# Optimization experiments

Measured on AMD Instinct MI355X. Metric: run time of the kernel, lower is better.

The kernel has to match this reference:

```python
import jax, jax.numpy as jnp
import numpy as np

D_MODEL = 1024
NUM_HEADS = 16
D_K = D_MODEL // NUM_HEADS


def setup_inputs() -> dict:
    key = jax.random.key(0)
    ks = jax.random.split(key, 7)
    B, S = 2, 2048
    scale = 1.0 / np.sqrt(D_MODEL)
    return {
        "Q": jax.random.normal(ks[0], (B, S, D_MODEL), dtype=jnp.float32),
        "K": jax.random.normal(ks[1], (B, S, D_MODEL), dtype=jnp.float32),
        "V": jax.random.normal(ks[2], (B, S, D_MODEL), dtype=jnp.float32),
        "W_q": jax.random.normal(ks[3], (D_MODEL, D_MODEL), dtype=jnp.float32) * scale,
        "W_k": jax.random.normal(ks[4], (D_MODEL, D_MODEL), dtype=jnp.float32) * scale,
        "W_v": jax.random.normal(ks[5], (D_MODEL, D_MODEL), dtype=jnp.float32) * scale,
        "W_o": jax.random.normal(ks[6], (D_MODEL, D_MODEL), dtype=jnp.float32) * scale,
    }


def _split_heads(x):
    B, S, _ = x.shape
    return x.reshape(B, S, NUM_HEADS, D_K).transpose(0, 2, 1, 3)  # [B,H,S,Dk]


def reference(Q, K, V, W_q, W_k, W_v, W_o):
    # nn.Linear(bias=False): x @ W.T
    q = _split_heads(Q @ W_q.T)
    k = _split_heads(K @ W_k.T)
    v = _split_heads(V @ W_v.T)
    scores = jnp.einsum("bhqd,bhkd->bhqk", q, k) / jnp.sqrt(jnp.float32(D_K))
    probs = jax.nn.softmax(scores, axis=-1)
    out = jnp.einsum("bhqk,bhkd->bhqd", probs, v)  # [B,H,S,Dk]
    B, H, S, Dk = out.shape
    out = out.transpose(0, 2, 1, 3).reshape(B, S, H * Dk)
    return out @ W_o.T
```

## Files before the change

### kernel.cpp

```cpp
#include <hip/hip_runtime.h>
#include <cstdint>

#define D_MODEL 1024
#define NH 16
#define DK 64
#define SEQ 2048
#define BATCH 2
#define M_TOT (BATCH * SEQ)

typedef __bf16 bf16x8          __attribute__((ext_vector_type(8)));
typedef unsigned short u16x8   __attribute__((ext_vector_type(8)));
typedef float  f32x4           __attribute__((ext_vector_type(4)));

union pun8 { u16x8 u; bf16x8 b; };

__device__ __forceinline__ f32x4 mfma16(bf16x8 a, bf16x8 b, f32x4 c) {
    return __builtin_amdgcn_mfma_f32_16x16x32_bf16(a, b, c, 0, 0, 0);
}

__device__ __forceinline__ unsigned short f2bf(float f) {
    union { float f; uint32_t u; } v; v.f = f;
    uint32_t u = v.u;
    return (unsigned short)((u + 0x7FFFu + ((u >> 16) & 1u)) >> 16);
}

__device__ __forceinline__ unsigned short f2bf_trunc(float f) {
    union { float f; uint32_t u; } v; v.f = f;
    return (unsigned short)(v.u >> 16);
}

__device__ __forceinline__ void gl_lds16(const unsigned short* g, unsigned short* l) {
    __builtin_amdgcn_global_load_lds(
        (const __attribute__((address_space(1))) void*)g,
        (__attribute__((address_space(3))) void*)l, 16, 0, 0);
}

#define C_EXP2 0.1803368801111204f

__global__ __launch_bounds__(256) void convert_all_kernel(
    const float* __restrict__ Q,  const float* __restrict__ K,
    const float* __restrict__ V,  const float* __restrict__ Wq,
    const float* __restrict__ Wk, const float* __restrict__ Wv,
    const float* __restrict__ Wo,
    unsigned short* __restrict__ Qb,  unsigned short* __restrict__ Kb,
    unsigned short* __restrict__ Vb,  unsigned short* __restrict__ Wqb,
    unsigned short* __restrict__ Wkb, unsigned short* __restrict__ Wvb,
    unsigned short* __restrict__ Wob)
{
    int bid = blockIdx.x;
    const float* src; unsigned short* dst; int base;
    if (bid < 3 * 2048) {
        int r = bid >> 11;
        src  = (r == 0) ? Q  : (r == 1) ? K  : V;
        dst  = (r == 0) ? Qb : (r == 1) ? Kb : Vb;
        base = (bid & 2047) * 2048;
    } else {
        int u = bid - 3 * 2048;
        int r = u >> 9;
        src  = (r == 0) ? Wq  : (r == 1) ? Wk  : (r == 2) ? Wv  : Wo;
        dst  = (r == 0) ? Wqb : (r == 1) ? Wkb : (r == 2) ? Wvb : Wob;
        base = (u & 511) * 2048;
    }
    int i = base + threadIdx.x * 8;
    float4 a = *(const float4*)(src + i);
    float4 b = *(const float4*)(src + i + 4);
    u16x8 o;
    o[0] = f2bf(a.x); o[1] = f2bf(a.y); o[2] = f2bf(a.z); o[3] = f2bf(a.w);
    o[4] = f2bf(b.x); o[5] = f2bf(b.y); o[6] = f2bf(b.z); o[7] = f2bf(b.w);
    *(u16x8*)(dst + i) = o;
}

__global__ __launch_bounds__(256) void qkv_proj_kernel(
    const unsigned short* __restrict__ Q,
    const unsigned short* __restrict__ K,
    const unsigned short* __restrict__ V,
    const unsigned short* __restrict__ Wq,
    const unsigned short* __restrict__ Wk,
    const unsigned short* __restrict__ Wv,
    unsigned short* __restrict__ qb,
    unsigned short* __restrict__ kb,
    unsigned short* __restrict__ vtb)
{
    const int z = blockIdx.z;
    const unsigned short* A  = (z == 0) ? Q  : (z == 1) ? K  : V;
    const unsigned short* Bt = (z == 0) ? Wq : (z == 1) ? Wk : Wv;

    const int m0 = blockIdx.y * 128;
    const int n0 = blockIdx.x * 128;

    __shared__ __align__(16) unsigned short smem[128 * 136];
    unsigned short* As = smem;
    unsigned short* Bs = smem + 128 * 64;
    unsigned short* Cs = smem;

    const int t    = threadIdx.x;
    const int lane = t & 63;
    const int w    = t >> 6;
    const int l15  = lane & 15;
    const int quad = lane >> 4;
    const int wm   = (w >> 1) * 64;
    const int wn   = (w & 1) * 64;

    f32x4 acc[4][4] = {};

    for (int k0 = 0; k0 < D_MODEL; k0 += 64) {
        __syncthreads();
        #pragma unroll
        for (int i = 0; i < 4; i++) {
            int u   = t + i * 256;
            int row = u >> 3;
            int kc  = (u & 7) * 8;
            gl_lds16(&A [(m0 + row) * D_MODEL + k0 + kc], &As[(i * 256 + w * 64) * 8]);
            gl_lds16(&Bt[(n0 + row) * D_MODEL + k0 + kc], &Bs[(i * 256 + w * 64) * 8]);
        }
        __syncthreads();

        #pragma unroll
        for (int kk = 0; kk < 2; kk++) {
            bf16x8 a[4], b[4];
            #pragma unroll
            for (int mi = 0; mi < 4; mi++)
                a[mi] = *(const bf16x8*)(&As[(wm + mi * 16 + l15) * 64 + kk * 32 + quad * 8]);
            #pragma unroll
            for (int ni = 0; ni < 4; ni++)
                b[ni] = *(const bf16x8*)(&Bs[(wn + ni * 16 + l15) * 64 + kk * 32 + quad * 8]);

            #pragma unroll
            for (int mi = 0; mi < 4; mi++)
                #pragma unroll
                for (int ni = 0; ni < 4; ni++)
                    acc[mi][ni] = mfma16(a[mi], b[ni], acc[mi][ni]);
        }
    }

    const float oscale = (z == 0) ? C_EXP2 : 1.0f;
    __syncthreads();
    #pragma unroll
    for (int mi = 0; mi < 4; mi++) {
        #pragma unroll
        for (int ni = 0; ni < 4; ni++) {
            #pragma unroll
            for (int r = 0; r < 4; r++) {
                int rloc = wm + mi * 16 + quad * 4 + r;
                int cloc = wn + ni * 16 + l15;
                int rr = (z == 2) ? cloc : rloc;
                int cc = (z == 2) ? rloc : cloc;
                Cs[rr * 136 + cc] = f2bf(acc[mi][ni][r] * oscale);
            }
        }
    }
    __syncthreads();
    #pragma unroll
    for (int i = 0; i < 8; i++) {
        int u    = t + i * 256;
        int rrow = u >> 4;
        int cc8  = (u & 15) * 8;
        u16x8 val = *(const u16x8*)(&Cs[rrow * 136 + cc8]);
        unsigned short* dst;
        if (z < 2) {
            int m = m0 + rrow, n = n0 + cc8;
            int bi = m >> 11, s = m & (SEQ - 1);
            int hh = n >> 6,  d = n & (DK - 1);
            dst = ((z == 0) ? qb : kb) + (((size_t)(bi * NH + hh) * SEQ + s) * DK + d);
        } else {
            int dglob = n0 + rrow;
            int bi = m0 >> 11, s = (m0 & (SEQ - 1)) + cc8;
            int hh = dglob >> 6, d = dglob & (DK - 1);
            dst = vtb + (((size_t)(bi * NH + hh) * DK + d) * SEQ + s);
        }
        *(u16x8*)dst = val;
    }
}

__global__ __launch_bounds__(512, 2) void attn_kernel(
    const unsigned short* __restrict__ qb,
    const unsigned short* __restrict__ kb,
    const unsigned short* __restrict__ vtb,
    unsigned short* __restrict__ ctx)
{
    const int h  = blockIdx.x;
    const int qt = blockIdx.y;
    const int b  = blockIdx.z;

    const int t    = threadIdx.x;
    const int lane = t & 63;
    const int w    = t >> 6;
    const int l15  = lane & 15;
    const int quad = lane >> 4;

    const unsigned short* qh = qb  + ((b * NH + h) * SEQ) * DK;
    const unsigned short* kh = kb  + ((b * NH + h) * SEQ) * DK;
    const unsigned short* vh = vtb + ((b * NH + h) * DK) * SEQ;

    __shared__ __align__(16) unsigned short p_lds[8][32][72];

    const int qrow0 = qt * 256 + w * 32;
    bf16x8 qa[2][2];
    #pragma unroll
    for (int m = 0; m < 2; m++)
        #pragma unroll
        for (int kk = 0; kk < 2; kk++)
            qa[m][kk] = *(const bf16x8*)(&qh[(qrow0 + m * 16 + l15) * DK + kk * 32 + quad * 8]);

    pun8 ones_p;
    #pragma unroll
    for (int i = 0; i < 8; i++) ones_p.u[i] = 0x3F80;
    const bf16x8 ones = ones_p.b;

    f32x4 o[2][4] = {};
    f32x4 lacc[2] = {};

    for (int kt = 0; kt < SEQ / 128; kt++) {
        #pragma unroll
        for (int hh = 0; hh < 2; hh++) {
            const int kvbase = kt * 128 + hh * 64;

            bf16x8 kf[4][2];
            #pragma unroll
            for (int nb = 0; nb < 4; nb++) {
                const int krow = kvbase + nb * 16 + l15;
                kf[nb][0] = *(const bf16x8*)(&kh[krow * DK + quad * 8]);
                kf[nb][1] = *(const bf16x8*)(&kh[krow * DK + 32 + quad * 8]);
            }

            f32x4 sacc[2][4] = {};
            __builtin_amdgcn_s_setprio(1);
            #pragma unroll
            for (int m = 0; m < 2; m++)
                #pragma unroll
                for (int nb = 0; nb < 4; nb++) {
                    sacc[m][nb] = mfma16(qa[m][0], kf[nb][0], sacc[m][nb]);
                    sacc[m][nb] = mfma16(qa[m][1], kf[nb][1], sacc[m][nb]);
                }
            __builtin_amdgcn_s_setprio(0);

            bf16x8 vf[4][2];
            #pragma unroll
            for (int db = 0; db < 4; db++) {
                const int vrow = (db * 16 + l15) * SEQ + kvbase;
                vf[db][0] = *(const bf16x8*)(&vh[vrow + quad * 8]);
                vf[db][1] = *(const bf16x8*)(&vh[vrow + 32 + quad * 8]);
            }

            #pragma unroll
            for (int m = 0; m < 2; m++)
                #pragma unroll
                for (int nb = 0; nb < 4; nb++)
                    #pragma unroll
                    for (int r = 0; r < 4; r++) {
                        float p = exp2f(sacc[m][nb][r]);
                        p_lds[w][m * 16 + quad * 4 + r][nb * 16 + l15] = f2bf_trunc(p);
                    }

            asm volatile("" ::: "memory");

            bf16x8 pa[2][2];
            #pragma unroll
            for (int m = 0; m < 2; m++)
                #pragma unroll
                for (int kk = 0; kk < 2; kk++)
                    pa[m][kk] = *(const bf16x8*)(&p_lds[w][m * 16 + l15][kk * 32 + quad * 8]);

            asm volatile("" ::: "memory");

            __builtin_amdgcn_s_setprio(1);
            #pragma unroll
            for (int db = 0; db < 4; db++)
                #pragma unroll
                for (int m = 0; m < 2; m++) {
                    o[m][db] = mfma16(pa[m][0], vf[db][0], o[m][db]);
                    o[m][db] = mfma16(pa[m][1], vf[db][1], o[m][db]);
                }

            #pragma unroll
            for (int m = 0; m < 2; m++) {
                lacc[m] = mfma16(pa[m][0], ones, lacc[m]);
                lacc[m] = mfma16(pa[m][1], ones, lacc[m]);
            }
            __builtin_amdgcn_s_setprio(0);
        }
    }

    #pragma unroll
    for (int m = 0; m < 2; m++) {
        const int srow_base = b * SEQ + qt * 256 + w * 32 + m * 16 + quad * 4;
        #pragma unroll
        for (int db = 0; db < 4; db++)
            #pragma unroll
            for (int r = 0; r < 4; r++) {
                float val = o[m][db][r] / lacc[m][r];
                ctx[(srow_base + r) * D_MODEL + h * DK + db * 16 + l15] = f2bf(val);
            }
    }
}

__global__ __launch_bounds__(256) void out_proj_kernel(
    const unsigned short* __restrict__ A,
    const unsigned short* __restrict__ Bt,
    float* __restrict__ out)
{
    const int m0 = blockIdx.y * 64;
    const int n0 = blockIdx.x * 128;

    __shared__ __align__(16) unsigned short As[64 * 64];
    __shared__ __align__(16) unsigned short Bs[128 * 64];

    const int t    = threadIdx.x;
    const int lane = t & 63;
    const int w    = t >> 6;
    const int l15  = lane & 15;
    const int quad = lane >> 4;
    const int wn   = w * 32;

    f32x4 acc[4][2] = {};

    for (int k0 = 0; k0 < D_MODEL; k0 += 64) {
        __syncthreads();
        #pragma unroll
        for (int i = 0; i < 2; i++) {
            int u   = t + i * 256;
            int row = u >> 3;
            int kc  = (u & 7) * 8;
            gl_lds16(&A[(m0 + row) * D_MODEL + k0 + kc], &As[(i * 256 + w * 64) * 8]);
        }
        #pragma unroll
        for (int i = 0; i < 4; i++) {
            int u   = t + i * 256;
            int row = u >> 3;
            int kc  = (u & 7) * 8;
            gl_lds16(&Bt[(n0 + row) * D_MODEL + k0 + kc], &Bs[(i * 256 + w * 64) * 8]);
        }
        __syncthreads();

        #pragma unroll
        for (int kk = 0; kk < 2; kk++) {
            bf16x8 a[4], bfr[2];
            #pragma unroll
            for (int mi = 0; mi < 4; mi++)
                a[mi] = *(const bf16x8*)(&As[(mi * 16 + l15) * 64 + kk * 32 + quad * 8]);
            #pragma unroll
            for (int ni = 0; ni < 2; ni++)
                bfr[ni] = *(const bf16x8*)(&Bs[(wn + ni * 16 + l15) * 64 + kk * 32 + quad * 8]);

            #pragma unroll
            for (int mi = 0; mi < 4; mi++)
                #pragma unroll
                for (int ni = 0; ni < 2; ni++)
                    acc[mi][ni] = mfma16(a[mi], bfr[ni], acc[mi][ni]);
        }
    }

    #pragma unroll
    for (int mi = 0; mi < 4; mi++) {
        #pragma unroll
        for (int ni = 0; ni < 2; ni++) {
            #pragma unroll
            for (int r = 0; r < 4; r++) {
                int m = m0 + mi * 16 + quad * 4 + r;
                int n = n0 + wn + ni * 16 + l15;
                out[m * D_MODEL + n] = acc[mi][ni][r];
            }
        }
    }
}

extern "C" void kernel_launch(void* const* d_in, const int* in_sizes, int n_in,
                              void* d_out, int out_size, void* d_ws, size_t ws_size,
                              hipStream_t stream) {
    const float* Q  = (const float*)d_in[0];
    const float* K  = (const float*)d_in[1];
    const float* V  = (const float*)d_in[2];
    const float* Wq = (const float*)d_in[3];
    const float* Wk = (const float*)d_in[4];
    const float* Wv = (const float*)d_in[5];
    const float* Wo = (const float*)d_in[6];

    const size_t NQ = (size_t)M_TOT * D_MODEL;
    const size_t NW = (size_t)D_MODEL * D_MODEL;

    unsigned short* Qb  = (unsigned short*)d_ws;
    unsigned short* Kb  = Qb  + NQ;
    unsigned short* Vb  = Kb  + NQ;
    unsigned short* Wqb = Vb  + NQ;
    unsigned short* Wkb = Wqb + NW;
    unsigned short* Wvb = Wkb + NW;
    unsigned short* Wob = Wvb + NW;
    unsigned short* qb  = Wob + NW;
    unsigned short* kbf = qb  + NQ;
    unsigned short* vtb = kbf + NQ;
    unsigned short* ctx = vtb + NQ;
    float* out = (float*)d_out;

    convert_all_kernel<<<3 * 2048 + 4 * 512, 256, 0, stream>>>(
        Q, K, V, Wq, Wk, Wv, Wo, Qb, Kb, Vb, Wqb, Wkb, Wvb, Wob);

    dim3 g1(D_MODEL / 128, M_TOT / 128, 3);
    qkv_proj_kernel<<<g1, 256, 0, stream>>>(Qb, Kb, Vb, Wqb, Wkb, Wvb, qb, kbf, vtb);

    dim3 g2(NH, SEQ / 256, BATCH);
    attn_kernel<<<g2, 512, 0, stream>>>(qb, kbf, vtb, ctx);

    dim3 g3(D_MODEL / 128, M_TOT / 64, 1);
    out_proj_kernel<<<g3, 256, 0, stream>>>(ctx, Wob, out);
}
```

Before: 282.8 us.

## Split attention KV range across two warp groups with LDS-staged K/V tiles

```diff
diff --git a/kernel.cpp b/kernel.cpp
--- a/kernel.cpp
+++ b/kernel.cpp
@@ -172,7 +172,7 @@
     }
 }
 
-__global__ __launch_bounds__(512, 2) void attn_kernel(
+__global__ __launch_bounds__(512, 4) void attn_kernel(
     const unsigned short* __restrict__ qb,
     const unsigned short* __restrict__ kb,
     const unsigned short* __restrict__ vtb,
@@ -185,16 +185,24 @@
     const int t    = threadIdx.x;
     const int lane = t & 63;
     const int w    = t >> 6;
+    const int g    = w >> 2;
+    const int wq   = w & 3;
     const int l15  = lane & 15;
     const int quad = lane >> 4;
+    const int tl   = t & 255;
 
     const unsigned short* qh = qb  + ((b * NH + h) * SEQ) * DK;
     const unsigned short* kh = kb  + ((b * NH + h) * SEQ) * DK;
     const unsigned short* vh = vtb + ((b * NH + h) * DK) * SEQ;
 
-    __shared__ __align__(16) unsigned short p_lds[8][32][72];
-
-    const int qrow0 = qt * 256 + w * 32;
+    __shared__ __align__(16) unsigned short smem[34816];
+    unsigned short* Ks = smem + g * 4352;
+    unsigned short* Vs = smem + 8704 + g * 4352;
+    unsigned short* Pw = smem + 17408 + w * 2176;
+    float* o_comb = (float*)smem;
+    float* l_comb = (float*)(smem + 17408);
+
+    const int qrow0 = qt * 128 + wq * 32;
     bf16x8 qa[2][2];
     #pragma unroll
     for (int m = 0; m < 2; m++)
@@ -210,87 +218,121 @@
     f32x4 o[2][4] = {};
     f32x4 lacc[2] = {};
 
-    for (int kt = 0; kt < SEQ / 128; kt++) {
-        #pragma unroll
-        for (int hh = 0; hh < 2; hh++) {
-            const int kvbase = kt * 128 + hh * 64;
-
-            bf16x8 kf[4][2];
+    for (int kt = 0; kt < 16; kt++) {
+        const int c64 = (g * 16 + kt) * 64;
+        __syncthreads();
+        #pragma unroll
+        for (int i = 0; i < 2; i++) {
+            int u   = tl + i * 256;
+            int row = u >> 3;
+            int c8  = (u & 7) * 8;
+            *(u16x8*)(&Ks[row * 68 + c8]) =
+                *(const u16x8*)(&kh[(c64 + row) * DK + c8]);
+        }
+        #pragma unroll
+        for (int i = 0; i < 2; i++) {
+            int u   = tl + i * 256;
+            int row = u >> 3;
+            int c8  = (u & 7) * 8;
+            *(u16x8*)(&Vs[row * 68 + c8]) =
+                *(const u16x8*)(&vh[row * SEQ + c64 + c8]);
+        }
+        __syncthreads();
+
+        bf16x8 kf[4][2];
+        #pragma unroll
+        for (int nb = 0; nb < 4; nb++) {
+            kf[nb][0] = *(const bf16x8*)(&Ks[(nb * 16 + l15) * 68 + quad * 8]);
+            kf[nb][1] = *(const bf16x8*)(&Ks[(nb * 16 + l15) * 68 + 32 + quad * 8]);
+        }
+
+        f32x4 sacc[2][4] = {};
+        __builtin_amdgcn_s_setprio(1);
+        #pragma unroll
+        for (int m = 0; m < 2; m++)
             #pragma unroll
             for (int nb = 0; nb < 4; nb++) {
-                const int krow = kvbase + nb * 16 + l15;
-                kf[nb][0] = *(const bf16x8*)(&kh[krow * DK + quad * 8]);
-                kf[nb][1] = *(const bf16x8*)(&kh[krow * DK + 32 + quad * 8]);
+                sacc[m][nb] = mfma16(qa[m][0], kf[nb][0], sacc[m][nb]);
+                sacc[m][nb] = mfma16(qa[m][1], kf[nb][1], sacc[m][nb]);
             }
-
-            f32x4 sacc[2][4] = {};
-            __builtin_amdgcn_s_setprio(1);
-            #pragma unroll
-            for (int m = 0; m < 2; m++)
-                #pragma unroll
-                for (int nb = 0; nb < 4; nb++) {
-                    sacc[m][nb] = mfma16(qa[m][0], kf[nb][0], sacc[m][nb]);
-                    sacc[m][nb] = mfma16(qa[m][1], kf[nb][1], sacc[m][nb]);
+        __builtin_amdgcn_s_setprio(0);
+
+        #pragma unroll
+        for (int m = 0; m < 2; m++)
+            #pragma unroll
+            for (int nb = 0; nb < 4; nb++)
+                #pragma unroll
+                for (int r = 0; r < 4; r++) {
+                    float p = exp2f(sacc[m][nb][r]);
+                    Pw[(m * 16 + quad * 4 + r) * 68 + nb * 16 + l15] = f2bf_trunc(p);
                 }
-            __builtin_amdgcn_s_setprio(0);
-
-            bf16x8 vf[4][2];
-            #pragma unroll
-            for (int db = 0; db < 4; db++) {
-                const int vrow = (db * 16 + l15) * SEQ + kvbase;
-                vf[db][0] = *(const bf16x8*)(&vh[vrow + quad * 8]);
-                vf[db][1] = *(const bf16x8*)(&vh[vrow + 32 + quad * 8]);
+
+        asm volatile("" ::: "memory");
+
+        bf16x8 pa[2][2];
+        #pragma unroll
+        for (int m = 0; m < 2; m++)
+            #pragma unroll
+            for (int kk = 0; kk < 2; kk++)
+                pa[m][kk] = *(const bf16x8*)(&Pw[(m * 16 + l15) * 68 + kk * 32 + quad * 8]);
+
+        asm volatile("" ::: "memory");
+
+        bf16x8 vf[4][2];
+        #pragma unroll
+        for (int db = 0; db < 4; db++) {
+            vf[db][0] = *(const bf16x8*)(&Vs[(db * 16 + l15) * 68 + quad * 8]);
+            vf[db][1] = *(const bf16x8*)(&Vs[(db * 16 + l15) * 68 + 32 + quad * 8]);
+        }
+
+        __builtin_amdgcn_s_setprio(1);
+        #pragma unroll
+        for (int db = 0; db < 4; db++)
+            #pragma unroll
+            for (int m = 0; m < 2; m++) {
+                o[m][db] = mfma16(pa[m][0], vf[db][0], o[m][db]);
+                o[m][db] = mfma16(pa[m][1], vf[db][1], o[m][db]);
             }
-
-            #pragma unroll
-            for (int m = 0; m < 2; m++)
-                #pragma unroll
-                for (int nb = 0; nb < 4; nb++)
-                    #pragma unroll
-                    for (int r = 0; r < 4; r++) {
-                        float p = exp2f(sacc[m][nb][r]);
-                        p_lds[w][m * 16 + quad * 4 + r][nb * 16 + l15] = f2bf_trunc(p);
-                    }
-
-            asm volatile("" ::: "memory");
-
-            bf16x8 pa[2][2];
-            #pragma unroll
-            for (int m = 0; m < 2; m++)
-                #pragma unroll
-                for (int kk = 0; kk < 2; kk++)
-                    pa[m][kk] = *(const bf16x8*)(&p_lds[w][m * 16 + l15][kk * 32 + quad * 8]);
-
-            asm volatile("" ::: "memory");
-
-            __builtin_amdgcn_s_setprio(1);
+        #pragma unroll
+        for (int m = 0; m < 2; m++) {
+            lacc[m] = mfma16(pa[m][0], ones, lacc[m]);
+            lacc[m] = mfma16(pa[m][1], ones, lacc[m]);
+        }
+        __builtin_amdgcn_s_setprio(0);
+    }
+
+    __syncthreads();
+    if (g == 1) {
+        #pragma unroll
+        for (int m = 0; m < 2; m++) {
             #pragma unroll
             for (int db = 0; db < 4; db++)
                 #pragma unroll
-                for (int m = 0; m < 2; m++) {
-                    o[m][db] = mfma16(pa[m][0], vf[db][0], o[m][db]);
-                    o[m][db] = mfma16(pa[m][1], vf[db][1], o[m][db]);
+                for (int r = 0; r < 4; r++)
+                    o_comb[(wq * 32 + m * 16 + quad * 4 + r) * 64 + db * 16 + l15] =
+                        o[m][db][r];
+            if (l15 == 0) {
+                #pragma unroll
+                for (int r = 0; r < 4; r++)
+                    l_comb[wq * 32 + m * 16 + quad * 4 + r] = lacc[m][r];
+            }
+        }
+    }
+    __syncthreads();
+    if (g == 0) {
+        #pragma unroll
+        for (int m = 0; m < 2; m++) {
+            #pragma unroll
+            for (int db = 0; db < 4; db++)
+                #pragma unroll
+                for (int r = 0; r < 4; r++) {
+                    const int row_l = wq * 32 + m * 16 + quad * 4 + r;
+                    float val = (o[m][db][r] + o_comb[row_l * 64 + db * 16 + l15]) /
+                                (lacc[m][r] + l_comb[row_l]);
+                    ctx[(b * SEQ + qt * 128 + row_l) * D_MODEL + h * DK + db * 16 + l15] =
+                        f2bf(val);
                 }
-
-            #pragma unroll
-            for (int m = 0; m < 2; m++) {
-                lacc[m] = mfma16(pa[m][0], ones, lacc[m]);
-                lacc[m] = mfma16(pa[m][1], ones, lacc[m]);
-            }
-            __builtin_amdgcn_s_setprio(0);
-        }
-    }
-
-    #pragma unroll
-    for (int m = 0; m < 2; m++) {
-        const int srow_base = b * SEQ + qt * 256 + w * 32 + m * 16 + quad * 4;
-        #pragma unroll
-        for (int db = 0; db < 4; db++)
-            #pragma unroll
-            for (int r = 0; r < 4; r++) {
-                float val = o[m][db][r] / lacc[m][r];
-                ctx[(srow_base + r) * D_MODEL + h * DK + db * 16 + l15] = f2bf(val);
-            }
+        }
     }
 }
 
@@ -397,7 +439,7 @@
     dim3 g1(D_MODEL / 128, M_TOT / 128, 3);
     qkv_proj_kernel<<<g1, 256, 0, stream>>>(Qb, Kb, Vb, Wqb, Wkb, Wvb, qb, kbf, vtb);
 
-    dim3 g2(NH, SEQ / 256, BATCH);
+    dim3 g2(NH, SEQ / 128, BATCH);
     attn_kernel<<<g2, 512, 0, stream>>>(qb, kbf, vtb, ctx);
 
     dim3 g3(D_MODEL / 128, M_TOT / 64, 1);
```

Measured after the change: 349.1 us. +23.5%, slower.
